# Performance work log

Measured on AMD Instinct MI355X. Metric: run time of the kernel, lower is better.

## Reference

```python
import jax, jax.numpy as jnp
import numpy as np

N_LEVELS = 16
F_PER_LEVEL = 2
LOG2_T = 19
TABLE_SIZE = 1 << LOG2_T
BASE_RES = 16
MAX_RES = 4096
GEO_FEAT = 15
N_PTS = 524288

_b = np.exp((np.log(MAX_RES) - np.log(BASE_RES)) / (N_LEVELS - 1))
RES = np.floor(BASE_RES * _b ** np.arange(N_LEVELS)).astype(np.float32)  # [L]
PRIMES = np.array([1, 2654435761, 805459861], dtype=np.uint32)
# 8 trilinear corner offsets
OFFS = np.array([[(i >> 2) & 1, (i >> 1) & 1, i & 1] for i in range(8)], dtype=np.int32)


def hash_encode(x, table):
    # x: [N,3] in [0,1], table: [L,T,F]
    pos = x[None, :, :] * jnp.asarray(RES)[:, None, None]          # [L,N,3]
    p0 = jnp.floor(pos)
    frac = pos - p0                                                 # [L,N,3]
    corners = p0.astype(jnp.uint32)[:, :, None, :] + jnp.asarray(OFFS.astype(np.uint32))  # [L,N,8,3]
    hp = corners * jnp.asarray(PRIMES)                              # uint32 mul (wraps)
    h = (hp[..., 0] ^ hp[..., 1] ^ hp[..., 2]) & jnp.uint32(TABLE_SIZE - 1)  # [L,N,8]
    w = jnp.where(jnp.asarray(OFFS, bool), frac[:, :, None, :], 1.0 - frac[:, :, None, :]).prod(-1)  # [L,N,8]
    feats = jax.vmap(lambda t, i: t[i])(table, h)                   # [L,N,8,F] hashed gather
    out = (w[..., None] * feats).sum(axis=2)                        # [L,N,F]
    return out.transpose(1, 0, 2).reshape(x.shape[0], N_LEVELS * F_PER_LEVEL)  # [N,32]


def setup_inputs() -> dict:
    key = jax.random.key(0)
    ks = jax.random.split(key, 9)
    positions = jax.random.uniform(ks[0], (N_PTS, 3), dtype=jnp.float32)
    aabb = jnp.array([-1.0, -1.0, -1.0, 1.0, 1.0, 1.0], dtype=jnp.float32)
    table = jax.random.uniform(ks[1], (N_LEVELS, TABLE_SIZE, F_PER_LEVEL), minval=-1e-4, maxval=1e-4, dtype=jnp.float32)
    def lin(k, fan_in, fan_out):
        bound = 1.0 / np.sqrt(fan_in)
        kw, kb = jax.random.split(k)
        return (jax.random.uniform(kw, (fan_in, fan_out), minval=-bound, maxval=bound, dtype=jnp.float32),
                jax.random.uniform(kb, (fan_out,), minval=-bound, maxval=bound, dtype=jnp.float32))
    w1, b1 = lin(ks[2], 32, 64)
    w2, b2 = lin(ks[3], 64, 1 + GEO_FEAT)
    hw1, hb1 = lin(ks[4], GEO_FEAT, 64)
    hw2, hb2 = lin(ks[5], 64, 64)
    hw3, hb3 = lin(ks[6], 64, 3)
    return {"positions": positions, "aabb": aabb, "table": table,
            "w1": w1, "b1": b1, "w2": w2, "b2": b2,
            "hw1": hw1, "hb1": hb1, "hw2": hw2, "hb2": hb2, "hw3": hw3, "hb3": hb3}


def reference(positions, aabb, table, w1, b1, w2, b2, hw1, hb1, hw2, hb2, hw3, hb3):
    aabb_min, aabb_max = aabb[:3], aabb[3:]
    x = (positions - aabb_min) / (aabb_max - aabb_min)              # -> [0,1]
    selector = ((x > 0.0) & (x < 1.0)).all(axis=-1)                 # [N]
    enc = hash_encode(x, table)                                     # [N,32]
    h = jax.nn.relu(enc @ w1 + b1)                                  # [N,64]
    base = h @ w2 + b2                                              # [N,16]
    density_before = base[:, :1]
    embedding = base[:, 1:]
    density = jnp.exp(density_before - 1.0) * selector[:, None].astype(base.dtype)  # trunc_exp(x-1)
    hh = jax.nn.relu(embedding @ hw1 + hb1)
    hh = jax.nn.relu(hh @ hw2 + hb2)
    rgb = jax.nn.sigmoid(hh @ hw3 + hb3)                            # [N,3]
    return rgb, density
```

## Files before the change

### kernel.cpp

```cpp
#include <hip/hip_runtime.h>
#include <math.h>

#define NLV 16
#define TBLBITS 19
#define TBLMASK ((1u << TBLBITS) - 1u)

typedef __attribute__((ext_vector_type(8))) short bf16x8;
typedef __attribute__((ext_vector_type(4))) float f32x4;

__device__ __forceinline__ unsigned f2bf(float f) {
    unsigned u = __builtin_bit_cast(unsigned, f);
    return (u + 0x7fffu + ((u >> 16) & 1u)) >> 16;
}

__global__ __launch_bounds__(256)
void enc_kernel(const float* __restrict__ positions,
                const float* __restrict__ aabb,
                const float* __restrict__ table,
                unsigned* __restrict__ encOut, int npts,
                float r0_, float r1_, float r2_, float r3_,
                float r4_, float r5_, float r6_, float r7_,
                float r8_, float r9_, float r10_, float r11_,
                float r12_, float r13_, float r14_, float r15_)
{
    const unsigned l = blockIdx.y;
    const unsigned p = blockIdx.x * 256u + threadIdx.x;

    const bool s0 = (l & 1u), s1 = (l & 2u), s2 = (l & 4u), s3 = (l & 8u);
    float a0 = s0 ? r1_  : r0_;
    float a1 = s0 ? r3_  : r2_;
    float a2 = s0 ? r5_  : r4_;
    float a3 = s0 ? r7_  : r6_;
    float a4 = s0 ? r9_  : r8_;
    float a5 = s0 ? r11_ : r10_;
    float a6 = s0 ? r13_ : r12_;
    float a7 = s0 ? r15_ : r14_;
    float c0 = s1 ? a1 : a0;
    float c1 = s1 ? a3 : a2;
    float c2 = s1 ? a5 : a4;
    float c3 = s1 ? a7 : a6;
    float d0 = s2 ? c1 : c0;
    float d1 = s2 ? c3 : c2;
    const float r = s3 ? d1 : d0;

    const float px = positions[p * 3 + 0];
    const float py = positions[p * 3 + 1];
    const float pz = positions[p * 3 + 2];
    const float mnx = aabb[0], mny = aabb[1], mnz = aabb[2];
    const float mxx = aabb[3], mxy = aabb[4], mxz = aabb[5];
    const float x0 = (px - mnx) / (mxx - mnx);
    const float x1 = (py - mny) / (mxy - mny);
    const float x2 = (pz - mnz) / (mxz - mnz);

    const float fx = x0 * r, fy = x1 * r, fz = x2 * r;
    const float gx = floorf(fx), gy = floorf(fy), gz = floorf(fz);
    const unsigned cx = (unsigned)gx, cy = (unsigned)gy, cz = (unsigned)gz;
    const float rx = fx - gx, ry = fy - gy, rz = fz - gz;

    const float* tl = table + ((size_t)l << 20);
    float e0 = 0.f, e1 = 0.f;
    #pragma unroll
    for (int c = 0; c < 8; ++c) {
        const unsigned hx = cx + ((c >> 2) & 1);
        const unsigned hy = cy + ((c >> 1) & 1);
        const unsigned hz = cz + (c & 1);
        const unsigned h = (hx ^ hy * 2654435761u ^ hz * 805459861u) & TBLMASK;
        const float wx = (c & 4) ? rx : 1.f - rx;
        const float wy = (c & 2) ? ry : 1.f - ry;
        const float wz = (c & 1) ? rz : 1.f - rz;
        const float wgt = wx * wy * wz;
        const float2 f = *reinterpret_cast<const float2*>(tl + ((size_t)h << 1));
        e0 = fmaf(wgt, f.x, e0);
        e1 = fmaf(wgt, f.y, e1);
    }
    encOut[(size_t)l * npts + p] = f2bf(e0) | (f2bf(e1) << 16);
}

__global__ __launch_bounds__(256)
void prep_weights(const float* __restrict__ w1, const float* __restrict__ w2,
                  const float* __restrict__ hw1, const float* __restrict__ hw2,
                  const float* __restrict__ hw3, unsigned short* __restrict__ wt)
{
    for (int i = threadIdx.x; i < 12032; i += 256) {
        float v = 0.f;
        if (i < 2560) {
            int n = i / 40, k = i % 40;
            if (k < 32) v = w1[k * 64 + n];
        } else if (i < 5120) {
            int j = i - 2560, n = j / 40, k = j % 40;
            if (k < 15) v = hw1[k * 64 + n];
        } else if (i < 6272) {
            int j = i - 5120, n = j / 72, k = j % 72;
            if (k < 64) v = w2[k * 16 + n];
        } else if (i < 10880) {
            int j = i - 6272, n = j / 72, k = j % 72;
            if (k < 64) v = hw2[k * 64 + n];
        } else {
            int j = i - 10880, n = j / 72, k = j % 72;
            if (k < 64 && n < 3) v = hw3[k * 3 + n];
        }
        wt[i] = (unsigned short)f2bf(v);
    }
}

__global__ __launch_bounds__(256)
void mlp_kernel(const unsigned* __restrict__ enc,
                const unsigned short* __restrict__ wt,
                const float* __restrict__ positions,
                const float* __restrict__ aabb,
                const float* __restrict__ b1, const float* __restrict__ b2,
                const float* __restrict__ hb1, const float* __restrict__ hb2,
                const float* __restrict__ hb3,
                float* __restrict__ out, int npts)
{
    __shared__ __align__(16) unsigned short H[4][64 * 72];
    __shared__ float sel_lds[256];

    const int tid  = threadIdx.x;
    const int wave = tid >> 6;
    const int lane = tid & 63;
    const int col  = lane & 15;
    const int lgrp = lane >> 4;
    const int blockPt = blockIdx.x * 256;

    {
        const int gp = blockPt + tid;
        const float px = positions[gp * 3 + 0];
        const float py = positions[gp * 3 + 1];
        const float pz = positions[gp * 3 + 2];
        const float mnx = aabb[0], mny = aabb[1], mnz = aabb[2];
        const float mxx = aabb[3], mxy = aabb[4], mxz = aabb[5];
        const float x0 = (px - mnx) / (mxx - mnx);
        const float x1 = (py - mny) / (mxy - mny);
        const float x2 = (pz - mnz) / (mxz - mnz);
        const bool sel = (x0 > 0.f) && (x0 < 1.f) && (x1 > 0.f) && (x1 < 1.f) &&
                         (x2 > 0.f) && (x2 < 1.f);
        sel_lds[tid] = sel ? 1.f : 0.f;
    }

    float bias1[4], biasH1[4], biasH2[4];
    #pragma unroll
    for (int nt = 0; nt < 4; ++nt) {
        bias1[nt]  = b1[nt * 16 + col];
        biasH1[nt] = hb1[nt * 16 + col];
        biasH2[nt] = hb2[nt * 16 + col];
    }
    const float bias2 = b2[col];
    float biasH3 = 0.f;
    if (col < 3) biasH3 = hb3[col];

    bf16x8 a1[4];
    #pragma unroll
    for (int mt = 0; mt < 4; ++mt) {
        const int ptl = blockPt + wave * 64 + mt * 16 + col;
        uint4 v;
        v.x = enc[(size_t)(lgrp * 4 + 0) * npts + ptl];
        v.y = enc[(size_t)(lgrp * 4 + 1) * npts + ptl];
        v.z = enc[(size_t)(lgrp * 4 + 2) * npts + ptl];
        v.w = enc[(size_t)(lgrp * 4 + 3) * npts + ptl];
        a1[mt] = __builtin_bit_cast(bf16x8, v);
    }

    const unsigned short* w1t = wt;
    const unsigned short* w3t = wt + 2560;
    const unsigned short* w2t = wt + 5120;
    const unsigned short* w4t = wt + 6272;
    const unsigned short* w5t = wt + 10880;
    unsigned short* Hw = H[wave];

    const f32x4 zero = {0.f, 0.f, 0.f, 0.f};

    {
        f32x4 acc[4][4];
        #pragma unroll
        for (int mt = 0; mt < 4; ++mt)
            #pragma unroll
            for (int nt = 0; nt < 4; ++nt) acc[mt][nt] = zero;

        #pragma unroll
        for (int nt = 0; nt < 4; ++nt) {
            const bf16x8 b = *reinterpret_cast<const bf16x8*>(
                w1t + (nt * 16 + col) * 40 + lgrp * 8);
            #pragma unroll
            for (int mt = 0; mt < 4; ++mt)
                acc[mt][nt] = __builtin_amdgcn_mfma_f32_16x16x32_bf16(
                    a1[mt], b, acc[mt][nt], 0, 0, 0);
        }
        #pragma unroll
        for (int mt = 0; mt < 4; ++mt)
            #pragma unroll
            for (int nt = 0; nt < 4; ++nt)
                #pragma unroll
                for (int rr = 0; rr < 4; ++rr) {
                    const float h = fmaxf(acc[mt][nt][rr] + bias1[nt], 0.f);
                    const int row = mt * 16 + lgrp * 4 + rr;
                    Hw[row * 72 + nt * 16 + col] = (unsigned short)f2bf(h);
                }
    }

    {
        f32x4 acc[4];
        #pragma unroll
        for (int mt = 0; mt < 4; ++mt) acc[mt] = zero;

        #pragma unroll
        for (int ks = 0; ks < 2; ++ks) {
            const bf16x8 b = *reinterpret_cast<const bf16x8*>(
                w2t + col * 72 + ks * 32 + lgrp * 8);
            #pragma unroll
            for (int mt = 0; mt < 4; ++mt) {
                const bf16x8 a = *reinterpret_cast<const bf16x8*>(
                    Hw + (mt * 16 + col) * 72 + ks * 32 + lgrp * 8);
                acc[mt] = __builtin_amdgcn_mfma_f32_16x16x32_bf16(
                    a, b, acc[mt], 0, 0, 0);
            }
        }
        #pragma unroll
        for (int mt = 0; mt < 4; ++mt)
            #pragma unroll
            for (int rr = 0; rr < 4; ++rr) {
                const float base = acc[mt][rr] + bias2;
                const int row = mt * 16 + lgrp * 4 + rr;
                if (col == 0) {
                    const float dn =
                        expf(base - 1.f) * sel_lds[wave * 64 + row];
                    out[(size_t)npts * 3 + blockPt + wave * 64 + row] = dn;
                } else {
                    Hw[row * 72 + (col - 1)] = (unsigned short)f2bf(base);
                }
            }
        {
            const int row = lane;
            Hw[row * 72 + 15] = 0;
            const uint4 z4 = {0, 0, 0, 0};
            *reinterpret_cast<uint4*>(Hw + row * 72 + 16) = z4;
            *reinterpret_cast<uint4*>(Hw + row * 72 + 24) = z4;
        }
    }

    {
        f32x4 acc[4][4];
        #pragma unroll
        for (int mt = 0; mt < 4; ++mt)
            #pragma unroll
            for (int nt = 0; nt < 4; ++nt) acc[mt][nt] = zero;

        bf16x8 a[4];
        #pragma unroll
        for (int mt = 0; mt < 4; ++mt)
            a[mt] = *reinterpret_cast<const bf16x8*>(
                Hw + (mt * 16 + col) * 72 + lgrp * 8);

        #pragma unroll
        for (int nt = 0; nt < 4; ++nt) {
            const bf16x8 b = *reinterpret_cast<const bf16x8*>(
                w3t + (nt * 16 + col) * 40 + lgrp * 8);
            #pragma unroll
            for (int mt = 0; mt < 4; ++mt)
                acc[mt][nt] = __builtin_amdgcn_mfma_f32_16x16x32_bf16(
                    a[mt], b, acc[mt][nt], 0, 0, 0);
        }
        #pragma unroll
        for (int mt = 0; mt < 4; ++mt)
            #pragma unroll
            for (int nt = 0; nt < 4; ++nt)
                #pragma unroll
                for (int rr = 0; rr < 4; ++rr) {
                    const float h = fmaxf(acc[mt][nt][rr] + biasH1[nt], 0.f);
                    const int row = mt * 16 + lgrp * 4 + rr;
                    Hw[row * 72 + nt * 16 + col] = (unsigned short)f2bf(h);
                }
    }

    {
        f32x4 acc[4][4];
        #pragma unroll
        for (int mt = 0; mt < 4; ++mt)
            #pragma unroll
            for (int nt = 0; nt < 4; ++nt) acc[mt][nt] = zero;

        #pragma unroll
        for (int ks = 0; ks < 2; ++ks) {
            bf16x8 a[4];
            #pragma unroll
            for (int mt = 0; mt < 4; ++mt)
                a[mt] = *reinterpret_cast<const bf16x8*>(
                    Hw + (mt * 16 + col) * 72 + ks * 32 + lgrp * 8);
            #pragma unroll
            for (int nt = 0; nt < 4; ++nt) {
                const bf16x8 b = *reinterpret_cast<const bf16x8*>(
                    w4t + (nt * 16 + col) * 72 + ks * 32 + lgrp * 8);
                #pragma unroll
                for (int mt = 0; mt < 4; ++mt)
                    acc[mt][nt] = __builtin_amdgcn_mfma_f32_16x16x32_bf16(
                        a[mt], b, acc[mt][nt], 0, 0, 0);
            }
        }
        #pragma unroll
        for (int mt = 0; mt < 4; ++mt)
            #pragma unroll
            for (int nt = 0; nt < 4; ++nt)
                #pragma unroll
                for (int rr = 0; rr < 4; ++rr) {
                    const float h = fmaxf(acc[mt][nt][rr] + biasH2[nt], 0.f);
                    const int row = mt * 16 + lgrp * 4 + rr;
                    Hw[row * 72 + nt * 16 + col] = (unsigned short)f2bf(h);
                }
    }

    {
        f32x4 acc[4];
        #pragma unroll
        for (int mt = 0; mt < 4; ++mt) acc[mt] = zero;

        #pragma unroll
        for (int ks = 0; ks < 2; ++ks) {
            const bf16x8 b = *reinterpret_cast<const bf16x8*>(
                w5t + col * 72 + ks * 32 + lgrp * 8);
            #pragma unroll
            for (int mt = 0; mt < 4; ++mt) {
                const bf16x8 a = *reinterpret_cast<const bf16x8*>(
                    Hw + (mt * 16 + col) * 72 + ks * 32 + lgrp * 8);
                acc[mt] = __builtin_amdgcn_mfma_f32_16x16x32_bf16(
                    a, b, acc[mt], 0, 0, 0);
            }
        }
        if (col < 3) {
            #pragma unroll
            for (int mt = 0; mt < 4; ++mt)
                #pragma unroll
                for (int rr = 0; rr < 4; ++rr) {
                    const float v = acc[mt][rr] + biasH3;
                    const float rgb = 1.f / (1.f + expf(-v));
                    const int row = mt * 16 + lgrp * 4 + rr;
                    out[(size_t)(blockPt + wave * 64 + row) * 3 + col] = rgb;
                }
        }
    }
}

extern "C" void kernel_launch(void* const* d_in, const int* in_sizes, int n_in,
                              void* d_out, int out_size, void* d_ws, size_t ws_size,
                              hipStream_t stream) {
    const float* positions = (const float*)d_in[0];
    const float* aabb      = (const float*)d_in[1];
    const float* table     = (const float*)d_in[2];
    const float* w1  = (const float*)d_in[3];
    const float* b1  = (const float*)d_in[4];
    const float* w2  = (const float*)d_in[5];
    const float* b2  = (const float*)d_in[6];
    const float* hw1 = (const float*)d_in[7];
    const float* hb1 = (const float*)d_in[8];
    const float* hw2 = (const float*)d_in[9];
    const float* hb2 = (const float*)d_in[10];
    const float* hw3 = (const float*)d_in[11];
    const float* hb3 = (const float*)d_in[12];
    float* out = (float*)d_out;

    const int npts = in_sizes[0] / 3;

    unsigned* encbuf = (unsigned*)d_ws;
    unsigned short* wt =
        (unsigned short*)((char*)d_ws + (size_t)npts * 16 * 4);

    float R[NLV];
    const double bb = exp((log(4096.0) - log(16.0)) / 15.0);
    for (int l = 0; l < NLV; ++l)
        R[l] = (float)floor(16.0 * pow(bb, (double)l));

    dim3 egrid(npts / 256, NLV);
    enc_kernel<<<egrid, 256, 0, stream>>>(
        positions, aabb, table, encbuf, npts,
        R[0], R[1], R[2], R[3], R[4], R[5], R[6], R[7],
        R[8], R[9], R[10], R[11], R[12], R[13], R[14], R[15]);

    prep_weights<<<1, 256, 0, stream>>>(w1, w2, hw1, hw2, hw3, wt);

    mlp_kernel<<<npts / 256, 256, 0, stream>>>(
        encbuf, wt, positions, aabb, b1, b2, hb1, hb2, hb3, out, npts);
}
```

Before: 398.3 us.

## Pair x-neighbor hash gathers, halve MLP tile per wave, parallelize weight prep

```diff
diff --git a/kernel.cpp b/kernel.cpp
--- a/kernel.cpp
+++ b/kernel.cpp
@@ -4,6 +4,8 @@
 #define NLV 16
 #define TBLBITS 19
 #define TBLMASK ((1u << TBLBITS) - 1u)
+#define P2 2654435761u
+#define P3 805459861u
 
 typedef __attribute__((ext_vector_type(8))) short bf16x8;
 typedef __attribute__((ext_vector_type(4))) float f32x4;
@@ -59,19 +61,34 @@
 
     const float* tl = table + ((size_t)l << 20);
     float e0 = 0.f, e1 = 0.f;
+    const bool xeven = (cx & 1u) == 0u;
+
     #pragma unroll
-    for (int c = 0; c < 8; ++c) {
-        const unsigned hx = cx + ((c >> 2) & 1);
-        const unsigned hy = cy + ((c >> 1) & 1);
-        const unsigned hz = cz + (c & 1);
-        const unsigned h = (hx ^ hy * 2654435761u ^ hz * 805459861u) & TBLMASK;
-        const float wx = (c & 4) ? rx : 1.f - rx;
-        const float wy = (c & 2) ? ry : 1.f - ry;
-        const float wz = (c & 1) ? rz : 1.f - rz;
-        const float wgt = wx * wy * wz;
-        const float2 f = *reinterpret_cast<const float2*>(tl + ((size_t)h << 1));
-        e0 = fmaf(wgt, f.x, e0);
-        e1 = fmaf(wgt, f.y, e1);
+    for (int yz = 0; yz < 4; ++yz) {
+        const unsigned dy = (yz >> 1) & 1, dz = yz & 1;
+        const unsigned base = ((cy + dy) * P2) ^ ((cz + dz) * P3);
+        const float wy = dy ? ry : 1.f - ry;
+        const float wz = dz ? rz : 1.f - rz;
+        const float wyz = wy * wz;
+        const float wa = wyz * (1.f - rx);
+        const float wb = wyz * rx;
+        const unsigned i0 = (cx ^ base) & TBLMASK;
+
+        float f0x, f0y, f1x, f1y;
+        if (xeven) {
+            const float4 q = *reinterpret_cast<const float4*>(
+                tl + ((size_t)(i0 & ~1u) << 1));
+            const bool lo = (i0 & 1u) == 0u;
+            f0x = lo ? q.x : q.z;  f0y = lo ? q.y : q.w;
+            f1x = lo ? q.z : q.x;  f1y = lo ? q.w : q.y;
+        } else {
+            const unsigned i1 = ((cx + 1u) ^ base) & TBLMASK;
+            const float2 qa = *reinterpret_cast<const float2*>(tl + ((size_t)i0 << 1));
+            const float2 qb = *reinterpret_cast<const float2*>(tl + ((size_t)i1 << 1));
+            f0x = qa.x; f0y = qa.y; f1x = qb.x; f1y = qb.y;
+        }
+        e0 = fmaf(wa, f0x, e0); e0 = fmaf(wb, f1x, e0);
+        e1 = fmaf(wa, f0y, e1); e1 = fmaf(wb, f1y, e1);
     }
     encOut[(size_t)l * npts + p] = f2bf(e0) | (f2bf(e1) << 16);
 }
@@ -81,26 +98,26 @@
                   const float* __restrict__ hw1, const float* __restrict__ hw2,
                   const float* __restrict__ hw3, unsigned short* __restrict__ wt)
 {
-    for (int i = threadIdx.x; i < 12032; i += 256) {
-        float v = 0.f;
-        if (i < 2560) {
-            int n = i / 40, k = i % 40;
-            if (k < 32) v = w1[k * 64 + n];
-        } else if (i < 5120) {
-            int j = i - 2560, n = j / 40, k = j % 40;
-            if (k < 15) v = hw1[k * 64 + n];
-        } else if (i < 6272) {
-            int j = i - 5120, n = j / 72, k = j % 72;
-            if (k < 64) v = w2[k * 16 + n];
-        } else if (i < 10880) {
-            int j = i - 6272, n = j / 72, k = j % 72;
-            if (k < 64) v = hw2[k * 64 + n];
-        } else {
-            int j = i - 10880, n = j / 72, k = j % 72;
-            if (k < 64 && n < 3) v = hw3[k * 3 + n];
-        }
-        wt[i] = (unsigned short)f2bf(v);
-    }
+    const int i = blockIdx.x * 256 + threadIdx.x;
+    if (i >= 12032) return;
+    float v = 0.f;
+    if (i < 2560) {
+        int n = i / 40, k = i % 40;
+        if (k < 32) v = w1[k * 64 + n];
+    } else if (i < 5120) {
+        int j = i - 2560, n = j / 40, k = j % 40;
+        if (k < 15) v = hw1[k * 64 + n];
+    } else if (i < 6272) {
+        int j = i - 5120, n = j / 72, k = j % 72;
+        if (k < 64) v = w2[k * 16 + n];
+    } else if (i < 10880) {
+        int j = i - 6272, n = j / 72, k = j % 72;
+        if (k < 64) v = hw2[k * 64 + n];
+    } else {
+        int j = i - 10880, n = j / 72, k = j % 72;
+        if (k < 64 && n < 3) v = hw3[k * 3 + n];
+    }
+    wt[i] = (unsigned short)f2bf(v);
 }
 
 __global__ __launch_bounds__(256)
@@ -113,18 +130,19 @@
                 const float* __restrict__ hb3,
                 float* __restrict__ out, int npts)
 {
-    __shared__ __align__(16) unsigned short H[4][64 * 72];
-    __shared__ float sel_lds[256];
+    __shared__ __align__(16) unsigned short H[4][32 * 72];
+    __shared__ float sel_lds[128];
 
     const int tid  = threadIdx.x;
     const int wave = tid >> 6;
     const int lane = tid & 63;
     const int col  = lane & 15;
     const int lgrp = lane >> 4;
-    const int blockPt = blockIdx.x * 256;
-
-    {
-        const int gp = blockPt + tid;
+    const int blockPt = blockIdx.x * 128;
+    const int wavePt  = blockPt + wave * 32;
+
+    if (lane < 32) {
+        const int gp = wavePt + lane;
         const float px = positions[gp * 3 + 0];
         const float py = positions[gp * 3 + 1];
         const float pz = positions[gp * 3 + 2];
@@ -135,7 +153,7 @@
         const float x2 = (pz - mnz) / (mxz - mnz);
         const bool sel = (x0 > 0.f) && (x0 < 1.f) && (x1 > 0.f) && (x1 < 1.f) &&
                          (x2 > 0.f) && (x2 < 1.f);
-        sel_lds[tid] = sel ? 1.f : 0.f;
+        sel_lds[wave * 32 + lane] = sel ? 1.f : 0.f;
     }
 
     float bias1[4], biasH1[4], biasH2[4];
@@ -146,13 +164,12 @@
         biasH2[nt] = hb2[nt * 16 + col];
     }
     const float bias2 = b2[col];
-    float biasH3 = 0.f;
-    if (col < 3) biasH3 = hb3[col];
-
-    bf16x8 a1[4];
+    const float biasH3 = (col < 3) ? hb3[col] : 0.f;
+
+    bf16x8 a1[2];
     #pragma unroll
-    for (int mt = 0; mt < 4; ++mt) {
-        const int ptl = blockPt + wave * 64 + mt * 16 + col;
+    for (int mt = 0; mt < 2; ++mt) {
+        const int ptl = wavePt + mt * 16 + col;
         uint4 v;
         v.x = enc[(size_t)(lgrp * 4 + 0) * npts + ptl];
         v.y = enc[(size_t)(lgrp * 4 + 1) * npts + ptl];
@@ -168,47 +185,47 @@
     const unsigned short* w5t = wt + 10880;
     unsigned short* Hw = H[wave];
 
-    const f32x4 zero = {0.f, 0.f, 0.f, 0.f};
-
     {
-        f32x4 acc[4][4];
-        #pragma unroll
-        for (int mt = 0; mt < 4; ++mt)
-            #pragma unroll
-            for (int nt = 0; nt < 4; ++nt) acc[mt][nt] = zero;
-
+        f32x4 acc[2][4];
+        #pragma unroll
+        for (int mt = 0; mt < 2; ++mt)
+            #pragma unroll
+            for (int nt = 0; nt < 4; ++nt) {
+                const float b = bias1[nt];
+                acc[mt][nt] = (f32x4){b, b, b, b};
+            }
         #pragma unroll
         for (int nt = 0; nt < 4; ++nt) {
             const bf16x8 b = *reinterpret_cast<const bf16x8*>(
                 w1t + (nt * 16 + col) * 40 + lgrp * 8);
             #pragma unroll
-            for (int mt = 0; mt < 4; ++mt)
+            for (int mt = 0; mt < 2; ++mt)
                 acc[mt][nt] = __builtin_amdgcn_mfma_f32_16x16x32_bf16(
                     a1[mt], b, acc[mt][nt], 0, 0, 0);
         }
         #pragma unroll
-        for (int mt = 0; mt < 4; ++mt)
+        for (int mt = 0; mt < 2; ++mt)
             #pragma unroll
             for (int nt = 0; nt < 4; ++nt)
                 #pragma unroll
                 for (int rr = 0; rr < 4; ++rr) {
-                    const float h = fmaxf(acc[mt][nt][rr] + bias1[nt], 0.f);
+                    const float h = fmaxf(acc[mt][nt][rr], 0.f);
                     const int row = mt * 16 + lgrp * 4 + rr;
                     Hw[row * 72 + nt * 16 + col] = (unsigned short)f2bf(h);
                 }
     }
 
     {
-        f32x4 acc[4];
-        #pragma unroll
-        for (int mt = 0; mt < 4; ++mt) acc[mt] = zero;
-
+        f32x4 acc[2];
+        #pragma unroll
+        for (int mt = 0; mt < 2; ++mt)
+            acc[mt] = (f32x4){bias2, bias2, bias2, bias2};
         #pragma unroll
         for (int ks = 0; ks < 2; ++ks) {
             const bf16x8 b = *reinterpret_cast<const bf16x8*>(
                 w2t + col * 72 + ks * 32 + lgrp * 8);
             #pragma unroll
-            for (int mt = 0; mt < 4; ++mt) {
+            for (int mt = 0; mt < 2; ++mt) {
                 const bf16x8 a = *reinterpret_cast<const bf16x8*>(
                     Hw + (mt * 16 + col) * 72 + ks * 32 + lgrp * 8);
                 acc[mt] = __builtin_amdgcn_mfma_f32_16x16x32_bf16(
@@ -216,20 +233,19 @@
             }
         }
         #pragma unroll
-        for (int mt = 0; mt < 4; ++mt)
+        for (int mt = 0; mt < 2; ++mt)
             #pragma unroll
             for (int rr = 0; rr < 4; ++rr) {
-                const float base = acc[mt][rr] + bias2;
+                const float base = acc[mt][rr];
                 const int row = mt * 16 + lgrp * 4 + rr;
                 if (col == 0) {
-                    const float dn =
-                        expf(base - 1.f) * sel_lds[wave * 64 + row];
-                    out[(size_t)npts * 3 + blockPt + wave * 64 + row] = dn;
+                    const float dn = __expf(base - 1.f) * sel_lds[wave * 32 + row];
+                    out[(size_t)npts * 3 + wavePt + row] = dn;
                 } else {
                     Hw[row * 72 + (col - 1)] = (unsigned short)f2bf(base);
                 }
             }
-        {
+        if (lane < 32) {
             const int row = lane;
             Hw[row * 72 + 15] = 0;
             const uint4 z4 = {0, 0, 0, 0};
@@ -239,51 +255,54 @@
     }
 
     {
-        f32x4 acc[4][4];
-        #pragma unroll
-        for (int mt = 0; mt < 4; ++mt)
-            #pragma unroll
-            for (int nt = 0; nt < 4; ++nt) acc[mt][nt] = zero;
-
-        bf16x8 a[4];
-        #pragma unroll
-        for (int mt = 0; mt < 4; ++mt)
+        f32x4 acc[2][4];
+        #pragma unroll
+        for (int mt = 0; mt < 2; ++mt)
+            #pragma unroll
+            for (int nt = 0; nt < 4; ++nt) {
+                const float b = biasH1[nt];
+                acc[mt][nt] = (f32x4){b, b, b, b};
+            }
+        bf16x8 a[2];
+        #pragma unroll
+        for (int mt = 0; mt < 2; ++mt)
             a[mt] = *reinterpret_cast<const bf16x8*>(
                 Hw + (mt * 16 + col) * 72 + lgrp * 8);
-
         #pragma unroll
         for (int nt = 0; nt < 4; ++nt) {
             const bf16x8 b = *reinterpret_cast<const bf16x8*>(
                 w3t + (nt * 16 + col) * 40 + lgrp * 8);
             #pragma unroll
-            for (int mt = 0; mt < 4; ++mt)
+            for (int mt = 0; mt < 2; ++mt)
                 acc[mt][nt] = __builtin_amdgcn_mfma_f32_16x16x32_bf16(
                     a[mt], b, acc[mt][nt], 0, 0, 0);
         }
         #pragma unroll
-        for (int mt = 0; mt < 4; ++mt)
+        for (int mt = 0; mt < 2; ++mt)
             #pragma unroll
             for (int nt = 0; nt < 4; ++nt)
                 #pragma unroll
                 for (int rr = 0; rr < 4; ++rr) {
-                    const float h = fmaxf(acc[mt][nt][rr] + biasH1[nt], 0.f);
+                    const float h = fmaxf(acc[mt][nt][rr], 0.f);
                     const int row = mt * 16 + lgrp * 4 + rr;
                     Hw[row * 72 + nt * 16 + col] = (unsigned short)f2bf(h);
                 }
     }
 
     {
-        f32x4 acc[4][4];
-        #pragma unroll
-        for (int mt = 0; mt < 4; ++mt)
-            #pragma unroll
-            for (int nt = 0; nt < 4; ++nt) acc[mt][nt] = zero;
-
+        f32x4 acc[2][4];
+        #pragma unroll
+        for (int mt = 0; mt < 2; ++mt)
+            #pragma unroll
+            for (int nt = 0; nt < 4; ++nt) {
+                const float b = biasH2[nt];
+                acc[mt][nt] = (f32x4){b, b, b, b};
+            }
         #pragma unroll
         for (int ks = 0; ks < 2; ++ks) {
-            bf16x8 a[4];
-            #pragma unroll
-            for (int mt = 0; mt < 4; ++mt)
+            bf16x8 a[2];
+            #pragma unroll
+            for (int mt = 0; mt < 2; ++mt)
                 a[mt] = *reinterpret_cast<const bf16x8*>(
                     Hw + (mt * 16 + col) * 72 + ks * 32 + lgrp * 8);
             #pragma unroll
@@ -291,34 +310,34 @@
                 const bf16x8 b = *reinterpret_cast<const bf16x8*>(
                     w4t + (nt * 16 + col) * 72 + ks * 32 + lgrp * 8);
                 #pragma unroll
-                for (int mt = 0; mt < 4; ++mt)
+                for (int mt = 0; mt < 2; ++mt)
                     acc[mt][nt] = __builtin_amdgcn_mfma_f32_16x16x32_bf16(
                         a[mt], b, acc[mt][nt], 0, 0, 0);
             }
         }
         #pragma unroll
-        for (int mt = 0; mt < 4; ++mt)
+        for (int mt = 0; mt < 2; ++mt)
             #pragma unroll
             for (int nt = 0; nt < 4; ++nt)
                 #pragma unroll
                 for (int rr = 0; rr < 4; ++rr) {
-                    const float h = fmaxf(acc[mt][nt][rr] + biasH2[nt], 0.f);
+                    const float h = fmaxf(acc[mt][nt][rr], 0.f);
                     const int row = mt * 16 + lgrp * 4 + rr;
                     Hw[row * 72 + nt * 16 + col] = (unsigned short)f2bf(h);
                 }
     }
 
     {
-        f32x4 acc[4];
-        #pragma unroll
-        for (int mt = 0; mt < 4; ++mt) acc[mt] = zero;
-
+        f32x4 acc[2];
+        #pragma unroll
+        for (int mt = 0; mt < 2; ++mt)
+            acc[mt] = (f32x4){biasH3, biasH3, biasH3, biasH3};
         #pragma unroll
         for (int ks = 0; ks < 2; ++ks) {
             const bf16x8 b = *reinterpret_cast<const bf16x8*>(
                 w5t + col * 72 + ks * 32 + lgrp * 8);
             #pragma unroll
-            for (int mt = 0; mt < 4; ++mt) {
+            for (int mt = 0; mt < 2; ++mt) {
                 const bf16x8 a = *reinterpret_cast<const bf16x8*>(
                     Hw + (mt * 16 + col) * 72 + ks * 32 + lgrp * 8);
                 acc[mt] = __builtin_amdgcn_mfma_f32_16x16x32_bf16(
@@ -327,13 +346,13 @@
         }
         if (col < 3) {
             #pragma unroll
-            for (int mt = 0; mt < 4; ++mt)
+            for (int mt = 0; mt < 2; ++mt)
                 #pragma unroll
                 for (int rr = 0; rr < 4; ++rr) {
-                    const float v = acc[mt][rr] + biasH3;
-                    const float rgb = 1.f / (1.f + expf(-v));
+                    const float v = acc[mt][rr];
+                    const float rgb = 1.f / (1.f + __expf(-v));
                     const int row = mt * 16 + lgrp * 4 + rr;
-                    out[(size_t)(blockPt + wave * 64 + row) * 3 + col] = rgb;
+                    out[(size_t)(wavePt + row) * 3 + col] = rgb;
                 }
         }
     }
@@ -368,14 +387,14 @@
     for (int l = 0; l < NLV; ++l)
         R[l] = (float)floor(16.0 * pow(bb, (double)l));
 
+    prep_weights<<<47, 256, 0, stream>>>(w1, w2, hw1, hw2, hw3, wt);
+
     dim3 egrid(npts / 256, NLV);
     enc_kernel<<<egrid, 256, 0, stream>>>(
         positions, aabb, table, encbuf, npts,
         R[0], R[1], R[2], R[3], R[4], R[5], R[6], R[7],
         R[8], R[9], R[10], R[11], R[12], R[13], R[14], R[15]);
 
-    prep_weights<<<1, 256, 0, stream>>>(w1, w2, hw1, hw2, hw3, wt);
-
-    mlp_kernel<<<npts / 256, 256, 0, stream>>>(
+    mlp_kernel<<<npts / 128, 256, 0, stream>>>(
         encbuf, wt, positions, aabb, b1, b2, hb1, hb2, hb3, out, npts);
 }
```

After: 320.7 us. 19.5% less time.
